# Performance work log

Hardware: AMD Instinct MI355X
Metric: run time of the kernel (lower is better)

## Reference

```python
import jax, jax.numpy as jnp
import numpy as np

# DeepSeek-V3 MLA attention (q_lora_rank > 0 path), sdpa attn_type (causal)
B, S, DIM = 2, 2048, 2048
NH = 16
Q_LORA = 1536
KV_LORA = 512
NOPE = 128
ROPE = 64
VH = 128
QK_HD = NOPE + ROPE  # 192
EPS = 1e-6
SCALE = QK_HD ** -0.5
ROPE_THETA = 10000.0


def _freqs(seqlen, dim, base):
    f = 1.0 / base ** (np.arange(0, dim, 2, dtype=np.float32) / dim)
    ang = np.outer(np.arange(seqlen, dtype=np.float32), f)
    return jnp.asarray(np.cos(ang)), jnp.asarray(np.sin(ang))


def rmsnorm(x, w, eps=EPS):
    var = jnp.mean(jnp.square(x), axis=-1, keepdims=True)
    return x * jax.lax.rsqrt(var + eps) * w


def apply_rope(x, cos, sin):
    # x: [b, s, h, d]; cos/sin: [s, d//2]; interleaved complex pairs (x[2i], x[2i+1])
    xr, xi = x[..., 0::2], x[..., 1::2]
    c = cos[None, :, None, :]
    s = sin[None, :, None, :]
    yr = xr * c - xi * s
    yi = xr * s + xi * c
    return jnp.stack([yr, yi], axis=-1).reshape(x.shape)


def setup_inputs() -> dict:
    key = jax.random.key(0)
    ks = jax.random.split(key, 7)
    std = 0.02
    x = jax.random.normal(ks[0], (B, S, DIM), dtype=jnp.float32)
    cos, sin = _freqs(S, ROPE, ROPE_THETA)
    return {
        "x": x,
        "freqs_cos": cos,
        "freqs_sin": sin,
        "wq_a": jax.random.normal(ks[1], (DIM, Q_LORA), dtype=jnp.float32) * std,
        "q_norm_w": jnp.ones((Q_LORA,), dtype=jnp.float32),
        "wq_b": jax.random.normal(ks[2], (Q_LORA, NH * QK_HD), dtype=jnp.float32) * std,
        "wkv_a": jax.random.normal(ks[3], (DIM, KV_LORA + ROPE), dtype=jnp.float32) * std,
        "kv_norm_w": jnp.ones((KV_LORA,), dtype=jnp.float32),
        "wkv_b": jax.random.normal(ks[4], (KV_LORA, NH * (NOPE + VH)), dtype=jnp.float32) * std,
        "wo": jax.random.normal(ks[5], (NH * VH, DIM), dtype=jnp.float32) * std,
    }


def reference(x, freqs_cos, freqs_sin, wq_a, q_norm_w, wq_b, wkv_a, kv_norm_w, wkv_b, wo):
    b, s, _ = x.shape
    # low-rank Q projection: wq_a -> RMSNorm -> wq_b
    q = rmsnorm(x @ wq_a, q_norm_w) @ wq_b
    q = q.reshape(b, s, NH, QK_HD)
    q_nope, q_pe = q[..., :NOPE], q[..., NOPE:]
    q_pe = apply_rope(q_pe, freqs_cos, freqs_sin)
    q = jnp.concatenate([q_nope, q_pe], axis=-1)
    # low-rank KV: wkv_a -> split latent / rope part
    kv = x @ wkv_a
    kv_lat, k_pe = kv[..., :KV_LORA], kv[..., KV_LORA:]
    k_pe = apply_rope(k_pe[:, :, None, :], freqs_cos, freqs_sin)  # [b,s,1,ROPE]
    kv = rmsnorm(kv_lat, kv_norm_w) @ wkv_b
    kv = kv.reshape(b, s, NH, NOPE + VH)
    k_nope, v = kv[..., :NOPE], kv[..., NOPE:]
    k = jnp.concatenate([k_nope, jnp.broadcast_to(k_pe, (b, s, NH, ROPE))], axis=-1)
    # attention [b,h,s,d]
    q = q.transpose(0, 2, 1, 3)
    k = k.transpose(0, 2, 1, 3)
    v = v.transpose(0, 2, 1, 3)
    scores = jnp.einsum("bhqd,bhkd->bhqk", q, k) * SCALE
    causal = jnp.tril(jnp.ones((s, s), dtype=bool))
    scores = jnp.where(causal[None, None], scores, jnp.finfo(scores.dtype).min)
    probs = jax.nn.softmax(scores, axis=-1)
    out = jnp.einsum("bhqk,bhkd->bhqd", probs, v)
    out = out.transpose(0, 2, 1, 3).reshape(b, s, NH * VH)
    return out @ wo
```

## Files before the change

### kernel.cpp

```cpp
#include <hip/hip_runtime.h>
#include <cstdint>
#include <cstddef>

typedef __attribute__((ext_vector_type(8))) short bf16x8;
typedef __attribute__((ext_vector_type(4))) float f32x4;
typedef __attribute__((ext_vector_type(16))) float f32x16;

#define S_LEN 2048
#define SCALE2 0.10411754f

__device__ __forceinline__ ushort f2bf(float f) {
  uint32_t u = __float_as_uint(f);
  u = (u + 0x7FFFu + ((u >> 16) & 1u)) >> 16;
  return (ushort)u;
}
__device__ __forceinline__ float bf2f(ushort u) {
  return __uint_as_float(((uint32_t)u) << 16);
}

typedef __attribute__((address_space(1))) void GV;
typedef __attribute__((address_space(3))) void LV;
__device__ __forceinline__ void gload16(const void* g, void* l) {
  __builtin_amdgcn_global_load_lds((GV*)g, (LV*)l, 16, 0, 0);
}

__device__ __forceinline__ void store_out(float* p, float v) { *p = v; }
__device__ __forceinline__ void store_out(ushort* p, float v) { *p = f2bf(v); }

__global__ void k_f32_to_bf16(const float* __restrict__ in, ushort* __restrict__ out, int n4) {
  int i = blockIdx.x * blockDim.x + threadIdx.x;
  int stride = gridDim.x * blockDim.x;
  for (; i < n4; i += stride) {
    float4 v = reinterpret_cast<const float4*>(in)[i];
    ushort4 o;
    o.x = f2bf(v.x); o.y = f2bf(v.y); o.z = f2bf(v.z); o.w = f2bf(v.w);
    reinterpret_cast<ushort4*>(out)[i] = o;
  }
}

__global__ void k_transpose_f32_bf16(const float* __restrict__ in, ushort* __restrict__ out,
                                     int R, int C) {
  __shared__ float tile[32][33];
  int c0 = blockIdx.x * 32, r0 = blockIdx.y * 32;
  int tx = threadIdx.x, ty = threadIdx.y;
#pragma unroll
  for (int i = 0; i < 32; i += 8) {
    int r = r0 + ty + i, c = c0 + tx;
    if (r < R && c < C) tile[ty + i][tx] = in[(size_t)r * C + c];
  }
  __syncthreads();
#pragma unroll
  for (int i = 0; i < 32; i += 8) {
    int c = c0 + ty + i, r = r0 + tx;
    if (r < R && c < C) out[(size_t)c * R + r] = f2bf(tile[tx][ty + i]);
  }
}

template <typename OUT>
__global__ __launch_bounds__(256) void k_gemm(const ushort* __restrict__ A,
                                              const ushort* __restrict__ Bt,
                                              OUT* __restrict__ C, int K, int Nreal) {
  __shared__ ushort As[128 * 32];
  __shared__ ushort Bs[128 * 32];
  const int t = threadIdx.x, lane = t & 63, w = t >> 6;
  const int nwg = gridDim.x * gridDim.y;
  const int wg = blockIdx.y * gridDim.x + blockIdx.x;
  const int swz = (wg & 7) * (nwg >> 3) + (wg >> 3);
  const int m0 = (swz / gridDim.x) * 128, n0 = (swz % gridDim.x) * 128;
  const int wm = (w >> 1) * 64, wn = (w & 1) * 64;
  const int g = lane >> 4, q = lane & 15;
  f32x4 acc[4][4] = {};
  for (int kt = 0; kt < K; kt += 32) {
#pragma unroll
    for (int i = 0; i < 2; i++) {
      int idx = i * 256 + t;
      gload16(A + (size_t)(m0 + (idx >> 2)) * K + kt + (idx & 3) * 8,
              (char*)As + (size_t)(i * 256 + (w << 6)) * 16);
      gload16(Bt + (size_t)(n0 + (idx >> 2)) * K + kt + (idx & 3) * 8,
              (char*)Bs + (size_t)(i * 256 + (w << 6)) * 16);
    }
    __syncthreads();
    bf16x8 af[4], bfr[4];
#pragma unroll
    for (int mi = 0; mi < 4; mi++) af[mi] = *(const bf16x8*)(As + (wm + 16 * mi + q) * 32 + 8 * g);
#pragma unroll
    for (int ni = 0; ni < 4; ni++) bfr[ni] = *(const bf16x8*)(Bs + (wn + 16 * ni + q) * 32 + 8 * g);
#pragma unroll
    for (int mi = 0; mi < 4; mi++)
#pragma unroll
      for (int ni = 0; ni < 4; ni++)
        acc[mi][ni] = __builtin_amdgcn_mfma_f32_16x16x32_bf16(af[mi], bfr[ni], acc[mi][ni], 0, 0, 0);
    __syncthreads();
  }
#pragma unroll
  for (int mi = 0; mi < 4; mi++)
#pragma unroll
    for (int ni = 0; ni < 4; ni++) {
      int col = n0 + wn + 16 * ni + q;
      if (col < Nreal) {
        int row = m0 + wm + 16 * mi + 4 * g;
#pragma unroll
        for (int r = 0; r < 4; r++)
          store_out(&C[(size_t)(row + r) * Nreal + col], acc[mi][ni][r]);
      }
    }
}

__global__ __launch_bounds__(256) void k_gemm_kv(const ushort* __restrict__ A,
                                                 const ushort* __restrict__ Bt,
                                                 ushort* __restrict__ kbuf,
                                                 ushort* __restrict__ vT, int K) {
  __shared__ ushort As[128 * 32];
  __shared__ ushort Bs[128 * 32];
  const int t = threadIdx.x, lane = t & 63, w = t >> 6;
  const int nwg = gridDim.x * gridDim.y;
  const int wg = blockIdx.y * gridDim.x + blockIdx.x;
  const int swz = (wg & 7) * (nwg >> 3) + (wg >> 3);
  const int m0 = (swz / gridDim.x) * 128, n0 = (swz % gridDim.x) * 128;
  const int wm = (w >> 1) * 64, wn = (w & 1) * 64;
  const int g = lane >> 4, q = lane & 15;
  f32x4 acc[4][4] = {};
  for (int kt = 0; kt < K; kt += 32) {
#pragma unroll
    for (int i = 0; i < 2; i++) {
      int idx = i * 256 + t;
      gload16(A + (size_t)(m0 + (idx >> 2)) * K + kt + (idx & 3) * 8,
              (char*)As + (size_t)(i * 256 + (w << 6)) * 16);
      gload16(Bt + (size_t)(n0 + (idx >> 2)) * K + kt + (idx & 3) * 8,
              (char*)Bs + (size_t)(i * 256 + (w << 6)) * 16);
    }
    __syncthreads();
    bf16x8 af[4], bfr[4];
#pragma unroll
    for (int mi = 0; mi < 4; mi++) af[mi] = *(const bf16x8*)(As + (wm + 16 * mi + q) * 32 + 8 * g);
#pragma unroll
    for (int ni = 0; ni < 4; ni++) bfr[ni] = *(const bf16x8*)(Bs + (wn + 16 * ni + q) * 32 + 8 * g);
#pragma unroll
    for (int mi = 0; mi < 4; mi++)
#pragma unroll
      for (int ni = 0; ni < 4; ni++)
        acc[mi][ni] = __builtin_amdgcn_mfma_f32_16x16x32_bf16(af[mi], bfr[ni], acc[mi][ni], 0, 0, 0);
    __syncthreads();
  }
#pragma unroll
  for (int mi = 0; mi < 4; mi++)
#pragma unroll
    for (int ni = 0; ni < 4; ni++) {
      int col = n0 + wn + 16 * ni + q;
      int hh = col >> 8, jj = col & 255;
      int row0 = m0 + wm + 16 * mi + 4 * g;
#pragma unroll
      for (int r = 0; r < 4; r++) {
        int tok = row0 + r;
        int bb = tok >> 11, ss = tok & 2047;
        ushort v = f2bf(acc[mi][ni][r]);
        if (jj < 128)
          kbuf[((size_t)(bb * 16 + hh) * 2048 + ss) * 192 + jj] = v;
        else
          vT[((size_t)(bb * 16 + hh) * 128 + (jj - 128)) * 2048 + ss] = v;
      }
    }
}

__global__ void k_rmsnorm_bf16(const float* __restrict__ in, const float* __restrict__ w,
                               ushort* __restrict__ out, int D, int instride) {
  int row = blockIdx.x;
  const float* x = in + (size_t)row * instride;
  ushort* o = out + (size_t)row * D;
  float ss = 0.f;
  for (int i = threadIdx.x; i < D; i += 256) { float v = x[i]; ss += v * v; }
#pragma unroll
  for (int m = 1; m < 64; m <<= 1) ss += __shfl_xor(ss, m);
  __shared__ float red[4];
  if ((threadIdx.x & 63) == 0) red[threadIdx.x >> 6] = ss;
  __syncthreads();
  float tot = red[0] + red[1] + red[2] + red[3];
  float sc = rsqrtf(tot / (float)D + 1e-6f);
  for (int i = threadIdx.x; i < D; i += 256) o[i] = f2bf(x[i] * sc * w[i]);
}

__global__ void k_kvnorm_rope(const float* __restrict__ cqkv, const float* __restrict__ w,
                              const float* __restrict__ cosT, const float* __restrict__ sinT,
                              ushort* __restrict__ ckvn, ushort* __restrict__ kbuf) {
  int tok = blockIdx.x, b = tok >> 11, s = tok & 2047;
  const float* x = cqkv + (size_t)tok * 2112 + 1536;
  float ss = 0.f;
  for (int i = threadIdx.x; i < 512; i += 256) { float v = x[i]; ss += v * v; }
#pragma unroll
  for (int m = 1; m < 64; m <<= 1) ss += __shfl_xor(ss, m);
  __shared__ float red[4];
  if ((threadIdx.x & 63) == 0) red[threadIdx.x >> 6] = ss;
  __syncthreads();
  float tot = red[0] + red[1] + red[2] + red[3];
  float sc = rsqrtf(tot / 512.f + 1e-6f);
  for (int i = threadIdx.x; i < 512; i += 256) ckvn[(size_t)tok * 512 + i] = f2bf(x[i] * sc * w[i]);
  if (threadIdx.x < 32) {
    int i = threadIdx.x;
    float xr = x[512 + 2 * i], xi = x[512 + 2 * i + 1];
    float c = cosT[s * 32 + i], sn = sinT[s * 32 + i];
    uint32_t lo = f2bf(xr * c - xi * sn);
    uint32_t hi = f2bf(xr * sn + xi * c);
    uint32_t pk = lo | (hi << 16);
#pragma unroll
    for (int h = 0; h < 16; ++h)
      *(uint32_t*)(kbuf + ((size_t)(b * 16 + h) * 2048 + s) * 192 + 128 + 2 * i) = pk;
  }
}

__global__ void k_qrope(ushort* __restrict__ qb, const float* __restrict__ cosT,
                        const float* __restrict__ sinT) {
  int tok = blockIdx.x, s = tok & (S_LEN - 1);
  for (int pp = threadIdx.x; pp < 512; pp += 256) {
    int h = pp >> 5, i = pp & 31;
    ushort* base = qb + ((size_t)tok * 16 + h) * 192 + 128;
    float xr = bf2f(base[2 * i]), xi = bf2f(base[2 * i + 1]);
    float c = cosT[s * 32 + i], sn = sinT[s * 32 + i];
    base[2 * i] = f2bf(xr * c - xi * sn);
    base[2 * i + 1] = f2bf(xr * sn + xi * c);
  }
}

__global__ __launch_bounds__(256, 2) void k_attn7(const ushort* __restrict__ qb,
                                                  const ushort* __restrict__ kb,
                                                  const ushort* __restrict__ vT,
                                                  ushort* __restrict__ aout) {
  const int id = blockIdx.x;
  const int qt = 15 - (id >> 5);
  const int bh = id & 31;
  const int h = bh & 15, b = bh >> 4;

  const int t = threadIdx.x, lane = t & 63, w = t >> 6;
  const int lq = lane & 31, hi = lane >> 5;
  const int kx = (lq >> 3) & 3;

  __shared__ ushort Ks[2][6656];
  __shared__ ushort Vs[2][5120];

  const ushort* kh = kb + (size_t)(b * 16 + h) * (2048 * 192);
  const ushort* vh = vT + (size_t)(b * 16 + h) * (128 * 2048);

  auto stage = [&](int k0, int bi) {
#pragma unroll
    for (int it = 0; it < 4; ++it) {
      int ii = it * 4 + w;
      if (ii < 13) {
        unsigned s = ii * 64 + lane;
        int r = s / 25, cs = s - r * 25;
        if (r > 31) { r = 31; cs = 24; }
        int cg = cs ^ ((r >> 3) & 3);
        if (cg > 23) cg = 0;
        gload16(kh + (size_t)(k0 + r) * 192 + cg * 8, (char*)&Ks[bi][0] + ii * 1024);
      }
    }
#pragma unroll
    for (int it = 0; it < 3; ++it) {
      int ii = it * 4 + w;
      if (ii < 10) {
        unsigned s = ii * 64 + lane;
        int r = s / 5, cs = s - r * 5;
        int cg = cs ^ ((r >> 3) & 3);
        if (cg > 3) cg = 0;
        gload16(vh + (size_t)r * 2048 + k0 + cg * 8, (char*)&Vs[bi][0] + ii * 1024);
      }
    }
  };

  const int q0 = qt * 128;
  const int q0w = q0 + 32 * w;
  const int qg = q0w + lq;
  const int nkt = qt * 4 + 4;

  bf16x8 qf[12];
  {
    const ushort* qp = qb + ((size_t)(b * 2048 + qg) * 16 + h) * 192 + 8 * hi;
#pragma unroll
    for (int s = 0; s < 12; ++s) qf[s] = *(const bf16x8*)(qp + 16 * s);
  }

  f32x16 oacc[4];
#pragma unroll
  for (int db = 0; db < 4; ++db)
#pragma unroll
    for (int r = 0; r < 16; ++r) oacc[db][r] = 0.f;
  float m = -1e30f, l = 0.f;

  stage(0, 0);
  asm volatile("s_waitcnt vmcnt(0)" ::: "memory");
  __syncthreads();
  int cur = 0;

  for (int kt = 0; kt < nkt; ++kt) {
    const int k0 = kt * 32;
    if (kt + 1 < nkt) stage((kt + 1) * 32, cur ^ 1);
    const ushort* KB = &Ks[cur][0];
    const ushort* VB = &Vs[cur][0];
    if (k0 <= q0w + 31) {
      f32x16 sacc;
#pragma unroll
      for (int r = 0; r < 16; ++r) sacc[r] = 0.f;
      __builtin_amdgcn_s_setprio(1);
#pragma unroll
      for (int s = 0; s < 12; ++s) {
        bf16x8 kf = *(const bf16x8*)(KB + lq * 200 + (((2 * s + hi) ^ kx) << 3));
        sacc = __builtin_amdgcn_mfma_f32_32x32x16_bf16(kf, qf[s], sacc, 0, 0, 0);
      }
      __builtin_amdgcn_s_setprio(0);
      float sv[16];
#pragma unroll
      for (int r = 0; r < 16; ++r) sv[r] = sacc[r];
      if (k0 + 31 > q0w) {
#pragma unroll
        for (int r = 0; r < 16; ++r)
          if (k0 + (r & 3) + 8 * (r >> 2) + 4 * hi > qg) sv[r] = -1e30f;
      }
      float pmax = sv[0];
#pragma unroll
      for (int r = 1; r < 16; ++r) pmax = fmaxf(pmax, sv[r]);
      pmax = fmaxf(pmax, __shfl_xor(pmax, 32));
      float smax = pmax * SCALE2;
      if (!__all(smax - m <= 8.0f)) {
        float mnew = fmaxf(m, smax);
        float a = exp2f(m - mnew);
        l *= a;
#pragma unroll
        for (int db = 0; db < 4; ++db)
#pragma unroll
          for (int r = 0; r < 16; ++r) oacc[db][r] *= a;
        m = mnew;
      }
      float e[16]; float sum = 0.f;
#pragma unroll
      for (int r = 0; r < 16; ++r) { e[r] = exp2f(sv[r] * SCALE2 - m); sum += e[r]; }
      sum += __shfl_xor(sum, 32);
      l += sum;
      uint32_t pk[8];
#pragma unroll
      for (int i = 0; i < 8; ++i)
        pk[i] = (uint32_t)f2bf(e[2 * i]) | ((uint32_t)f2bf(e[2 * i + 1]) << 16);
      uint32_t sw[8];
#pragma unroll
      for (int i = 0; i < 8; ++i) sw[i] = (uint32_t)__shfl_xor((int)pk[i], 32);
      union { uint32_t u[4]; bf16x8 v; } p0, p1;
      p0.u[0] = hi ? sw[2] : pk[0];
      p0.u[1] = hi ? sw[3] : pk[1];
      p0.u[2] = hi ? pk[2] : sw[0];
      p0.u[3] = hi ? pk[3] : sw[1];
      p1.u[0] = hi ? sw[6] : pk[4];
      p1.u[1] = hi ? sw[7] : pk[5];
      p1.u[2] = hi ? pk[6] : sw[4];
      p1.u[3] = hi ? pk[7] : sw[5];
      __builtin_amdgcn_s_setprio(1);
#pragma unroll
      for (int db = 0; db < 4; ++db) {
        bf16x8 vf0 = *(const bf16x8*)(VB + (32 * db + lq) * 40 + ((hi ^ kx) << 3));
        bf16x8 vf1 = *(const bf16x8*)(VB + (32 * db + lq) * 40 + (((2 + hi) ^ kx) << 3));
        oacc[db] = __builtin_amdgcn_mfma_f32_32x32x16_bf16(vf0, p0.v, oacc[db], 0, 0, 0);
        oacc[db] = __builtin_amdgcn_mfma_f32_32x32x16_bf16(vf1, p1.v, oacc[db], 0, 0, 0);
      }
      __builtin_amdgcn_s_setprio(0);
    }
    asm volatile("s_waitcnt vmcnt(0) lgkmcnt(0)" ::: "memory");
    __syncthreads();
    cur ^= 1;
  }

  float inv = 1.f / l;
  ushort* op = aout + ((size_t)(b * 2048 + qg)) * 2048 + h * 128 + 4 * hi;
#pragma unroll
  for (int db = 0; db < 4; ++db)
#pragma unroll
    for (int i = 0; i < 8; ++i) {
      uint32_t u = (uint32_t)f2bf(oacc[db][2 * i] * inv) |
                   ((uint32_t)f2bf(oacc[db][2 * i + 1] * inv) << 16);
      int dbase = 32 * db + (i & 1) * 2 + (i >> 1) * 8;
      *(uint32_t*)(op + dbase) = u;
    }
}

extern "C" void kernel_launch(void* const* d_in, const int* in_sizes, int n_in,
                              void* d_out, int out_size, void* d_ws, size_t ws_size,
                              hipStream_t stream) {
  const float* x = (const float*)d_in[0];
  const float* fcos = (const float*)d_in[1];
  const float* fsin = (const float*)d_in[2];
  const float* wq_a = (const float*)d_in[3];
  const float* qnw = (const float*)d_in[4];
  const float* wq_b = (const float*)d_in[5];
  const float* wkv_a = (const float*)d_in[6];
  const float* kvnw = (const float*)d_in[7];
  const float* wkv_b = (const float*)d_in[8];
  const float* wo = (const float*)d_in[9];
  float* out = (float*)d_out;

  char* ws = (char*)d_ws;
  size_t off = 0;
  auto alloc = [&](size_t bytes) -> char* {
    char* p = ws + off;
    off += (bytes + 255) & ~(size_t)255;
    return p;
  };
  ushort* xb     = (ushort*)alloc(4096ull * 2048 * 2);
  ushort* wqkv_t = (ushort*)alloc(2176ull * 2048 * 2);
  ushort* wqb_t  = (ushort*)alloc(3072ull * 1536 * 2);
  ushort* wkvb_t = (ushort*)alloc(4096ull * 512 * 2);
  ushort* wo_t   = (ushort*)alloc(2048ull * 2048 * 2);
  float*  cqkv   = (float*)alloc(4096ull * 2112 * 4);
  ushort* cqn    = (ushort*)alloc(4096ull * 1536 * 2);
  ushort* ckvn   = (ushort*)alloc(4096ull * 512 * 2);
  ushort* kbuf   = (ushort*)alloc(2ull * 16 * 2048 * 192 * 2);
  ushort* qbuf   = (ushort*)cqkv;
  ushort* aout   = xb;
  ushort* vT     = wqkv_t;

  dim3 tb(32, 8);
  k_f32_to_bf16<<<2048, 256, 0, stream>>>(x, xb, 4096 * 2048 / 4);
  k_transpose_f32_bf16<<<dim3(48, 64), tb, 0, stream>>>(wq_a, wqkv_t, 2048, 1536);
  k_transpose_f32_bf16<<<dim3(18, 64), tb, 0, stream>>>(wkv_a, wqkv_t + 1536ull * 2048, 2048, 576);
  k_transpose_f32_bf16<<<dim3(96, 48), tb, 0, stream>>>(wq_b, wqb_t, 1536, 3072);
  k_transpose_f32_bf16<<<dim3(128, 16), tb, 0, stream>>>(wkv_b, wkvb_t, 512, 4096);
  k_transpose_f32_bf16<<<dim3(64, 64), tb, 0, stream>>>(wo, wo_t, 2048, 2048);

  k_gemm<float><<<dim3(17, 32), 256, 0, stream>>>(xb, wqkv_t, cqkv, 2048, 2112);

  k_rmsnorm_bf16<<<4096, 256, 0, stream>>>(cqkv, qnw, cqn, 1536, 2112);
  k_kvnorm_rope<<<4096, 256, 0, stream>>>(cqkv, kvnw, fcos, fsin, ckvn, kbuf);

  k_gemm<ushort><<<dim3(24, 32), 256, 0, stream>>>(cqn, wqb_t, qbuf, 1536, 3072);
  k_qrope<<<4096, 256, 0, stream>>>(qbuf, fcos, fsin);

  k_gemm_kv<<<dim3(32, 32), 256, 0, stream>>>(ckvn, wkvb_t, kbuf, vT, 512);

  k_attn7<<<dim3(512), 256, 0, stream>>>(qbuf, kbuf, vT, aout);

  k_gemm<float><<<dim3(16, 32), 256, 0, stream>>>(aout, wo_t, out, 2048, 2048);
}
```

Before: 401.0 us.

## Widen attention KV tile to 64 keys and drop double buffering

The attention kernel now processes 64 keys per iteration, with two score accumulators, instead of 32, which halves the number of loop iterations and barriers. It replaces the double-buffered LDS prefetch with a single buffer that is loaded synchronously at the start of each iteration. The V tile layout and its XOR swizzle are widened to suit the longer rows. This cuts per-iteration overhead and softmax rescale checks, but gives up the overlap of global loads with compute, so each tile's load latency is exposed.

```diff
diff --git a/kernel.cpp b/kernel.cpp
--- a/kernel.cpp
+++ b/kernel.cpp
@@ -220,10 +220,10 @@
   }
 }
 
-__global__ __launch_bounds__(256, 2) void k_attn7(const ushort* __restrict__ qb,
-                                                  const ushort* __restrict__ kb,
-                                                  const ushort* __restrict__ vT,
-                                                  ushort* __restrict__ aout) {
+__global__ __launch_bounds__(256, 2) void k_attn10(const ushort* __restrict__ qb,
+                                                   const ushort* __restrict__ kb,
+                                                   const ushort* __restrict__ vT,
+                                                   ushort* __restrict__ aout) {
   const int id = blockIdx.x;
   const int qt = 15 - (id >> 5);
   const int bh = id & 31;
@@ -233,34 +233,33 @@
   const int lq = lane & 31, hi = lane >> 5;
   const int kx = (lq >> 3) & 3;
 
-  __shared__ ushort Ks[2][6656];
-  __shared__ ushort Vs[2][5120];
+  __shared__ ushort Ks[64 * 200];
+  __shared__ ushort Vs[128 * 72];
 
   const ushort* kh = kb + (size_t)(b * 16 + h) * (2048 * 192);
   const ushort* vh = vT + (size_t)(b * 16 + h) * (128 * 2048);
 
-  auto stage = [&](int k0, int bi) {
-#pragma unroll
-    for (int it = 0; it < 4; ++it) {
+  auto stage = [&](int k0) {
+#pragma unroll
+    for (int it = 0; it < 7; ++it) {
       int ii = it * 4 + w;
-      if (ii < 13) {
+      if (ii < 25) {
         unsigned s = ii * 64 + lane;
-        int r = s / 25, cs = s - r * 25;
-        if (r > 31) { r = 31; cs = 24; }
-        int cg = cs ^ ((r >> 3) & 3);
+        int r = s / 25, e = s - r * 25;
+        int cg = e ^ ((r >> 3) & 3);
         if (cg > 23) cg = 0;
-        gload16(kh + (size_t)(k0 + r) * 192 + cg * 8, (char*)&Ks[bi][0] + ii * 1024);
-      }
-    }
-#pragma unroll
-    for (int it = 0; it < 3; ++it) {
+        gload16(kh + (size_t)(k0 + r) * 192 + cg * 8, (char*)Ks + ii * 1024);
+      }
+    }
+#pragma unroll
+    for (int it = 0; it < 5; ++it) {
       int ii = it * 4 + w;
-      if (ii < 10) {
+      if (ii < 18) {
         unsigned s = ii * 64 + lane;
-        int r = s / 5, cs = s - r * 5;
-        int cg = cs ^ ((r >> 3) & 3);
-        if (cg > 3) cg = 0;
-        gload16(vh + (size_t)r * 2048 + k0 + cg * 8, (char*)&Vs[bi][0] + ii * 1024);
+        int r = s / 9, e = s - r * 9;
+        int cg = e ^ ((r >> 3) & 7);
+        if (cg > 7) cg = 0;
+        gload16(vh + (size_t)r * 2048 + k0 + cg * 8, (char*)Vs + ii * 1024);
       }
     }
   };
@@ -268,7 +267,7 @@
   const int q0 = qt * 128;
   const int q0w = q0 + 32 * w;
   const int qg = q0w + lq;
-  const int nkt = qt * 4 + 4;
+  const int nkt = qt * 2 + 2;
 
   bf16x8 qf[12];
   {
@@ -284,38 +283,39 @@
     for (int r = 0; r < 16; ++r) oacc[db][r] = 0.f;
   float m = -1e30f, l = 0.f;
 
-  stage(0, 0);
-  asm volatile("s_waitcnt vmcnt(0)" ::: "memory");
-  __syncthreads();
-  int cur = 0;
-
   for (int kt = 0; kt < nkt; ++kt) {
-    const int k0 = kt * 32;
-    if (kt + 1 < nkt) stage((kt + 1) * 32, cur ^ 1);
-    const ushort* KB = &Ks[cur][0];
-    const ushort* VB = &Vs[cur][0];
+    const int k0 = kt * 64;
+    stage(k0);
+    asm volatile("s_waitcnt vmcnt(0)" ::: "memory");
+    __syncthreads();
     if (k0 <= q0w + 31) {
-      f32x16 sacc;
-#pragma unroll
-      for (int r = 0; r < 16; ++r) sacc[r] = 0.f;
+      f32x16 sA, sB;
+#pragma unroll
+      for (int r = 0; r < 16; ++r) { sA[r] = 0.f; sB[r] = 0.f; }
       __builtin_amdgcn_s_setprio(1);
 #pragma unroll
       for (int s = 0; s < 12; ++s) {
-        bf16x8 kf = *(const bf16x8*)(KB + lq * 200 + (((2 * s + hi) ^ kx) << 3));
-        sacc = __builtin_amdgcn_mfma_f32_32x32x16_bf16(kf, qf[s], sacc, 0, 0, 0);
+        int ch = ((2 * s + hi) ^ kx) << 3;
+        bf16x8 kfA = *(const bf16x8*)(Ks + lq * 200 + ch);
+        bf16x8 kfB = *(const bf16x8*)(Ks + (lq + 32) * 200 + ch);
+        sA = __builtin_amdgcn_mfma_f32_32x32x16_bf16(kfA, qf[s], sA, 0, 0, 0);
+        sB = __builtin_amdgcn_mfma_f32_32x32x16_bf16(kfB, qf[s], sB, 0, 0, 0);
       }
       __builtin_amdgcn_s_setprio(0);
-      float sv[16];
-#pragma unroll
-      for (int r = 0; r < 16; ++r) sv[r] = sacc[r];
-      if (k0 + 31 > q0w) {
-#pragma unroll
-        for (int r = 0; r < 16; ++r)
-          if (k0 + (r & 3) + 8 * (r >> 2) + 4 * hi > qg) sv[r] = -1e30f;
-      }
-      float pmax = sv[0];
-#pragma unroll
-      for (int r = 1; r < 16; ++r) pmax = fmaxf(pmax, sv[r]);
+      float svA[16], svB[16];
+#pragma unroll
+      for (int r = 0; r < 16; ++r) { svA[r] = sA[r]; svB[r] = sB[r]; }
+      if (k0 + 63 > q0w) {
+#pragma unroll
+        for (int r = 0; r < 16; ++r) {
+          int kk = (r & 3) + 8 * (r >> 2) + 4 * hi;
+          if (k0 + kk > qg) svA[r] = -1e30f;
+          if (k0 + 32 + kk > qg) svB[r] = -1e30f;
+        }
+      }
+      float pmax = fmaxf(svA[0], svB[0]);
+#pragma unroll
+      for (int r = 1; r < 16; ++r) pmax = fmaxf(pmax, fmaxf(svA[r], svB[r]));
       pmax = fmaxf(pmax, __shfl_xor(pmax, 32));
       float smax = pmax * SCALE2;
       if (!__all(smax - m <= 8.0f)) {
@@ -328,40 +328,63 @@
           for (int r = 0; r < 16; ++r) oacc[db][r] *= a;
         m = mnew;
       }
-      float e[16]; float sum = 0.f;
-#pragma unroll
-      for (int r = 0; r < 16; ++r) { e[r] = exp2f(sv[r] * SCALE2 - m); sum += e[r]; }
+      float eA[16], eB[16]; float sum = 0.f;
+#pragma unroll
+      for (int r = 0; r < 16; ++r) {
+        eA[r] = exp2f(svA[r] * SCALE2 - m);
+        eB[r] = exp2f(svB[r] * SCALE2 - m);
+        sum += eA[r] + eB[r];
+      }
       sum += __shfl_xor(sum, 32);
       l += sum;
-      uint32_t pk[8];
-#pragma unroll
-      for (int i = 0; i < 8; ++i)
-        pk[i] = (uint32_t)f2bf(e[2 * i]) | ((uint32_t)f2bf(e[2 * i + 1]) << 16);
-      uint32_t sw[8];
-#pragma unroll
-      for (int i = 0; i < 8; ++i) sw[i] = (uint32_t)__shfl_xor((int)pk[i], 32);
-      union { uint32_t u[4]; bf16x8 v; } p0, p1;
-      p0.u[0] = hi ? sw[2] : pk[0];
-      p0.u[1] = hi ? sw[3] : pk[1];
-      p0.u[2] = hi ? pk[2] : sw[0];
-      p0.u[3] = hi ? pk[3] : sw[1];
-      p1.u[0] = hi ? sw[6] : pk[4];
-      p1.u[1] = hi ? sw[7] : pk[5];
-      p1.u[2] = hi ? pk[6] : sw[4];
-      p1.u[3] = hi ? pk[7] : sw[5];
+      uint32_t pkA[8], pkB[8];
+#pragma unroll
+      for (int i = 0; i < 8; ++i) {
+        pkA[i] = (uint32_t)f2bf(eA[2 * i]) | ((uint32_t)f2bf(eA[2 * i + 1]) << 16);
+        pkB[i] = (uint32_t)f2bf(eB[2 * i]) | ((uint32_t)f2bf(eB[2 * i + 1]) << 16);
+      }
+      uint32_t swA[8], swB[8];
+#pragma unroll
+      for (int i = 0; i < 8; ++i) {
+        swA[i] = (uint32_t)__shfl_xor((int)pkA[i], 32);
+        swB[i] = (uint32_t)__shfl_xor((int)pkB[i], 32);
+      }
+      union { uint32_t u[4]; bf16x8 v; } pA0, pA1, pB0, pB1;
+      pA0.u[0] = hi ? swA[2] : pkA[0];
+      pA0.u[1] = hi ? swA[3] : pkA[1];
+      pA0.u[2] = hi ? pkA[2] : swA[0];
+      pA0.u[3] = hi ? pkA[3] : swA[1];
+      pA1.u[0] = hi ? swA[6] : pkA[4];
+      pA1.u[1] = hi ? swA[7] : pkA[5];
+      pA1.u[2] = hi ? pkA[6] : swA[4];
+      pA1.u[3] = hi ? pkA[7] : swA[5];
+      pB0.u[0] = hi ? swB[2] : pkB[0];
+      pB0.u[1] = hi ? swB[3] : pkB[1];
+      pB0.u[2] = hi ? pkB[2] : swB[0];
+      pB0.u[3] = hi ? pkB[3] : swB[1];
+      pB1.u[0] = hi ? swB[6] : pkB[4];
+      pB1.u[1] = hi ? swB[7] : pkB[5];
+      pB1.u[2] = hi ? pkB[6] : swB[4];
+      pB1.u[3] = hi ? pkB[7] : swB[5];
       __builtin_amdgcn_s_setprio(1);
 #pragma unroll
       for (int db = 0; db < 4; ++db) {
-        bf16x8 vf0 = *(const bf16x8*)(VB + (32 * db + lq) * 40 + ((hi ^ kx) << 3));
-        bf16x8 vf1 = *(const bf16x8*)(VB + (32 * db + lq) * 40 + (((2 + hi) ^ kx) << 3));
-        oacc[db] = __builtin_amdgcn_mfma_f32_32x32x16_bf16(vf0, p0.v, oacc[db], 0, 0, 0);
-        oacc[db] = __builtin_amdgcn_mfma_f32_32x32x16_bf16(vf1, p1.v, oacc[db], 0, 0, 0);
+        const int d = 32 * db + lq;
+        const int vx = (d >> 3) & 7;
+        const ushort* vr = Vs + d * 72;
+        bf16x8 vf0 = *(const bf16x8*)(vr + (((0 + hi) ^ vx) << 3));
+        bf16x8 vf1 = *(const bf16x8*)(vr + (((2 + hi) ^ vx) << 3));
+        bf16x8 vf2 = *(const bf16x8*)(vr + (((4 + hi) ^ vx) << 3));
+        bf16x8 vf3 = *(const bf16x8*)(vr + (((6 + hi) ^ vx) << 3));
+        oacc[db] = __builtin_amdgcn_mfma_f32_32x32x16_bf16(vf0, pA0.v, oacc[db], 0, 0, 0);
+        oacc[db] = __builtin_amdgcn_mfma_f32_32x32x16_bf16(vf1, pA1.v, oacc[db], 0, 0, 0);
+        oacc[db] = __builtin_amdgcn_mfma_f32_32x32x16_bf16(vf2, pB0.v, oacc[db], 0, 0, 0);
+        oacc[db] = __builtin_amdgcn_mfma_f32_32x32x16_bf16(vf3, pB1.v, oacc[db], 0, 0, 0);
       }
       __builtin_amdgcn_s_setprio(0);
     }
-    asm volatile("s_waitcnt vmcnt(0) lgkmcnt(0)" ::: "memory");
-    __syncthreads();
-    cur ^= 1;
+    asm volatile("s_waitcnt lgkmcnt(0)" ::: "memory");
+    __syncthreads();
   }
 
   float inv = 1.f / l;
@@ -430,7 +453,7 @@
 
   k_gemm_kv<<<dim3(32, 32), 256, 0, stream>>>(ckvn, wkvb_t, kbuf, vT, 512);
 
-  k_attn7<<<dim3(512), 256, 0, stream>>>(qbuf, kbuf, vT, aout);
+  k_attn10<<<dim3(512), 256, 0, stream>>>(qbuf, kbuf, vT, aout);
 
   k_gemm<float><<<dim3(16, 32), 256, 0, stream>>>(aout, wo_t, out, 2048, 2048);
 }
```

Result: faster. 388.1 us (-3.2%).
